# Kernel tuning notes

Measured on AMD Instinct MI355X. Metric: run time of the kernel, lower is better.

The kernel has to match this reference:

```python
import jax, jax.numpy as jnp
import numpy as np

N = 100_000          # nodes
E = 1_600_000        # directed edges
GENE_DIM = 39
NUM_CLASSES = 5
EPS = 1e-5           # BatchNorm1d eps
DIMS = [(GENE_DIM, 64), (64, 128), (128, 64), (64, 32)]


def setup_inputs() -> dict:
    key = jax.random.key(0)
    ks = jax.random.split(key, 32)
    inp = {
        "x": jax.random.normal(ks[0], (N, GENE_DIM), dtype=jnp.float32),
        "edge_index": jax.random.randint(ks[1], (2, E), 0, N, dtype=jnp.int64),
    }
    ki = 2
    for i, (din, dout) in enumerate(DIMS, start=1):
        scale = 1.0 / np.sqrt(din)
        inp[f"W{i}"] = jax.random.uniform(ks[ki], (din, dout), jnp.float32, -scale, scale); ki += 1
        inp[f"b{i}"] = jnp.zeros((dout,), jnp.float32)
        inp[f"g{i}"] = jnp.ones((dout,), jnp.float32)    # BN gamma
        inp[f"be{i}"] = jnp.zeros((dout,), jnp.float32)  # BN beta
    scale = 1.0 / np.sqrt(32)
    inp["Wc"] = jax.random.uniform(ks[ki], (32, NUM_CLASSES), jnp.float32, -scale, scale)
    inp["bc"] = jnp.zeros((NUM_CLASSES,), jnp.float32)
    return inp


def reference(x, edge_index,
              W1, b1, g1, be1,
              W2, b2, g2, be2,
              W3, b3, g3, be3,
              W4, b4, g4, be4,
              Wc, bc):
    n = x.shape[0]
    # --- self loops + symmetric GCN normalization (shared by all 4 convs) ---
    loop = jnp.arange(n, dtype=edge_index.dtype)
    src = jnp.concatenate([edge_index[0], loop])   # message source (x_j)
    dst = jnp.concatenate([edge_index[1], loop])   # aggregation target
    deg = jax.ops.segment_sum(jnp.ones_like(dst, dtype=x.dtype), dst, num_segments=n)
    dinv = jnp.where(deg > 0, jax.lax.rsqrt(deg), 0.0)
    norm = (dinv[src] * dinv[dst])[:, None]        # [E+n, 1]

    def conv(h, W, b):
        # linear transform, gather from source, normalize, scatter-add at target
        m = (h @ W)[src] * norm
        return jax.ops.segment_sum(m, dst, num_segments=n) + b

    def bn(h, g, be):
        # training-mode BatchNorm1d: biased variance over the node axis
        mu = jnp.mean(h, axis=0)
        var = jnp.mean(jnp.square(h - mu), axis=0)
        return g * (h - mu) * jax.lax.rsqrt(var + EPS) + be

    h = bn(jax.nn.relu(conv(x, W1, b1)), g1, be1)
    h = bn(jax.nn.relu(conv(h, W2, b2)), g2, be2)
    h = bn(jax.nn.relu(conv(h, W3, b3)), g3, be3)
    h = bn(jax.nn.relu(conv(h, W4, b4)), g4, be4)
    out = h @ Wc + bc
    return (out, h)
```

## Files before the change

kernel.cpp:

```cpp
#include <hip/hip_runtime.h>

typedef unsigned int uint;
typedef unsigned short ushort;
typedef __attribute__((ext_vector_type(8))) short bf16x8;
typedef __attribute__((ext_vector_type(4))) float f32x4;

#define N_NODES 100000
#define N_EDGES 1600000
#define NB_C 256
#define TILE_C ((N_EDGES + NB_C - 1) / NB_C)
#define NB_D ((N_NODES + 511) / 512)
#define MG_GRID ((N_NODES + 63) / 64)
#define AGG_GRID 2048
constexpr float BN_EPS = 1e-5f;

__device__ __forceinline__ float bflo(uint w) { return __uint_as_float(w << 16); }
__device__ __forceinline__ float bfhi(uint w) { return __uint_as_float(w & 0xffff0000u); }
__device__ __forceinline__ ushort f2bf(float x) {
    uint u = __float_as_uint(x);
    uint r = (u + 0x7fffu + ((u >> 16) & 1u)) >> 16;
    return (ushort)r;
}
__device__ __forceinline__ uint pack2(float a, float b) {
    return (uint)f2bf(a) | ((uint)f2bf(b) << 16);
}

__global__ void detect_kernel(const int* __restrict__ ep, int* __restrict__ flag)
{
    __shared__ int cnt;
    if (threadIdx.x == 0) cnt = 0;
    __syncthreads();
    int nz = 0;
    for (int k = threadIdx.x; k < 1024; k += blockDim.x)
        if (ep[2 * k + 1] != 0) nz++;
    atomicAdd(&cnt, nz);
    __syncthreads();
    if (threadIdx.x == 0) *flag = (cnt == 0) ? 1 : 0;
}

__global__ __launch_bounds__(256) void coarseA_kernel(const int* __restrict__ ep,
                                                      const int* __restrict__ flag,
                                                      uint* __restrict__ ch)
{
    __shared__ uint lh[256];
    int t = threadIdx.x, blk = blockIdx.x;
    lh[t] = 0;
    __syncthreads();
    bool i64 = (*flag != 0);
    int start = blk * TILE_C;
    int end = start + TILE_C;
    if (end > N_EDGES) end = N_EDGES;
    for (int e = start + t; e < end; e += 256) {
        int d = i64 ? ep[2 * (N_EDGES + e)] : ep[N_EDGES + e];
        atomicAdd(&lh[d >> 9], 1u);
    }
    __syncthreads();
    ch[t * NB_C + blk] = lh[t];
}

__global__ void scanB_kernel(uint* __restrict__ ch, uint* __restrict__ bucketBase)
{
    __shared__ uint tot[256];
    int t = threadIdx.x;
    uint s = 0;
    for (int i = 0; i < NB_C; i++) s += ch[t * NB_C + i];
    tot[t] = s;
    __syncthreads();
    for (int off = 1; off < 256; off <<= 1) {
        uint add = (t >= off) ? tot[t - off] : 0u;
        __syncthreads();
        tot[t] += add;
        __syncthreads();
    }
    uint base = tot[t] - s;
    bucketBase[t] = base;
    if (t == 255) bucketBase[256] = base + s;
    uint run = base;
    for (int i = 0; i < NB_C; i++) {
        uint c = ch[t * NB_C + i];
        ch[t * NB_C + i] = run;
        run += c;
    }
}

__global__ __launch_bounds__(256) void scatterC_kernel(const int* __restrict__ ep,
                                                       const int* __restrict__ flag,
                                                       const uint* __restrict__ ch,
                                                       int2* __restrict__ pair)
{
    __shared__ uint loff[256];
    int t = threadIdx.x, blk = blockIdx.x;
    loff[t] = ch[t * NB_C + blk];
    __syncthreads();
    bool i64 = (*flag != 0);
    int start = blk * TILE_C;
    int end = start + TILE_C;
    if (end > N_EDGES) end = N_EDGES;
    for (int e = start + t; e < end; e += 256) {
        int s, d;
        if (i64) { s = ep[2 * e]; d = ep[2 * (N_EDGES + e)]; }
        else     { s = ep[e];     d = ep[N_EDGES + e]; }
        uint pos = atomicAdd(&loff[d >> 9], 1u);
        pair[pos] = make_int2(s, d);
    }
}

__global__ __launch_bounds__(256) void bucketD_kernel(const int2* __restrict__ pair,
                                                      const uint* __restrict__ bucketBase,
                                                      int* __restrict__ rowptr,
                                                      float* __restrict__ dinv,
                                                      int* __restrict__ colidx)
{
    __shared__ uint cnt[512], offp[512], s2[256];
    int bin = blockIdx.x, t = threadIdx.x;
    cnt[t] = 0; cnt[t + 256] = 0;
    __syncthreads();
    uint lo = bucketBase[bin], hi = bucketBase[bin + 1];
    for (uint p = lo + t; p < hi; p += 256)
        atomicAdd(&cnt[pair[p].y & 511], 1u);
    __syncthreads();
    uint a = cnt[2 * t], b = cnt[2 * t + 1];
    s2[t] = a + b;
    __syncthreads();
    for (int off = 1; off < 256; off <<= 1) {
        uint add = (t >= off) ? s2[t - off] : 0u;
        __syncthreads();
        s2[t] += add;
        __syncthreads();
    }
    uint excl = s2[t] - (a + b);
    offp[2 * t] = excl;
    offp[2 * t + 1] = excl + a;
    __syncthreads();
    for (int k = t; k < 512; k += 256) {
        int d = bin * 512 + k;
        if (d < N_NODES) {
            rowptr[d] = (int)(lo + offp[k]);
            dinv[d] = rsqrtf((float)(cnt[k] + 1));
        }
    }
    if (bin == 0 && t == 0) rowptr[N_NODES] = N_EDGES;
    __syncthreads();
    for (uint p = lo + t; p < hi; p += 256) {
        int2 pr = pair[p];
        uint pos = lo + atomicAdd(&offp[pr.y & 511], 1u);
        colidx[pos] = pr.x;
    }
}

__global__ __launch_bounds__(256) void xscale_kernel(const float* __restrict__ x,
                                                     const float* __restrict__ dinv,
                                                     uint* __restrict__ xs)
{
    int idx = blockIdx.x * 256 + threadIdx.x;
    if (idx >= N_NODES * 32) return;
    int i = idx >> 5;
    int u = idx & 31;
    int c0 = 2 * u, c1 = 2 * u + 1;
    float di = dinv[i];
    float v0 = (c0 < 39) ? x[i * 39 + c0] * di : 0.f;
    float v1 = (c1 < 39) ? x[i * 39 + c1] * di : 0.f;
    xs[idx] = pack2(v0, v1);
}

__global__ void packW_kernel(const float* __restrict__ W, ushort* __restrict__ out,
                             int din, int dout, int K)
{
    int CT = dout >> 4;
    int tot = (K >> 5) * CT * 64 * 8;
    for (int idx = blockIdx.x * 256 + threadIdx.x; idx < tot; idx += gridDim.x * 256) {
        int j = idx & 7;
        int lane = (idx >> 3) & 63;
        int slot = idx >> 9;
        int ct = slot % CT, kt = slot / CT;
        int k = kt * 32 + (lane >> 4) * 8 + j;
        int c = ct * 16 + (lane & 15);
        float v = (k < din) ? W[k * dout + c] : 0.f;
        out[idx] = f2bf(v);
    }
}

__global__ __launch_bounds__(256) void rowsum_kernel(
    const int* __restrict__ rowptr, const int* __restrict__ colidx,
    const float* __restrict__ dinv, float* __restrict__ rowsumP)
{
    int tid = threadIdx.x;
    int lane = tid & 63, wid = tid >> 6;
    int g16 = lane >> 4, gl = lane & 15;
    int gid = (blockIdx.x * 4 + wid) * 4 + g16;
    int ng = gridDim.x * 16;
    for (int i0 = gid; i0 < N_NODES; i0 += ng) {
        int s0 = rowptr[i0], e0 = rowptr[i0 + 1];
        float ad = 0.f;
        for (int e = s0 + gl; e < e0; e += 16) ad += dinv[colidx[e]];
        ad += __shfl_xor(ad, 1); ad += __shfl_xor(ad, 2);
        ad += __shfl_xor(ad, 4); ad += __shfl_xor(ad, 8);
        if (gl == 0) {
            float di = dinv[i0];
            rowsumP[i0] = di * (ad + di);
        }
    }
}

template <int D, int MODE>
__global__ __launch_bounds__(256) void agg_kernel(
    const ushort* __restrict__ table, const int* __restrict__ rowptr,
    const int* __restrict__ colidx, const float* __restrict__ dinv,
    const float* __restrict__ bias,
    ushort* __restrict__ outB, float* __restrict__ outF,
    float* __restrict__ Psum, float* __restrict__ Psq)
{
    constexpr int LPE = D / 8;
    constexpr int S = 64 / LPE;
    int tid = threadIdx.x;
    int lane = tid & 63, wid = tid >> 6;
    int seg = lane & (LPE - 1);
    int slot = lane / LPE;
    const ushort* segbase = table + seg * 8;

    float bv[8];
    if constexpr (MODE >= 1) {
        float4 b0 = *(const float4*)&bias[seg * 8];
        float4 b1 = *(const float4*)&bias[seg * 8 + 4];
        bv[0] = b0.x; bv[1] = b0.y; bv[2] = b0.z; bv[3] = b0.w;
        bv[4] = b1.x; bv[5] = b1.y; bv[6] = b1.z; bv[7] = b1.w;
    }
    float lsum[8] = {}, lsq[8] = {};

    for (int i = blockIdx.x * 4 + wid; i < N_NODES; i += gridDim.x * 4) {
        int iu = __builtin_amdgcn_readfirstlane(i);
        int s0 = rowptr[iu], e0 = rowptr[iu + 1];
        float acc[8] = {};
        if (slot == 0) {
            const uint4 w = *(const uint4*)(segbase + (size_t)iu * D);
            acc[0] = bflo(w.x); acc[1] = bfhi(w.x);
            acc[2] = bflo(w.y); acc[3] = bfhi(w.y);
            acc[4] = bflo(w.z); acc[5] = bfhi(w.z);
            acc[6] = bflo(w.w); acc[7] = bfhi(w.w);
        }
        for (int eb = s0; eb < e0; eb += S) {
            int e = eb + slot;
            if (e < e0) {
                int j = colidx[e];
                const uint4 w = *(const uint4*)(segbase + (size_t)j * D);
                acc[0] += bflo(w.x); acc[1] += bfhi(w.x);
                acc[2] += bflo(w.y); acc[3] += bfhi(w.y);
                acc[4] += bflo(w.z); acc[5] += bfhi(w.z);
                acc[6] += bflo(w.w); acc[7] += bfhi(w.w);
            }
        }
#pragma unroll
        for (int m = LPE; m < 64; m <<= 1) {
#pragma unroll
            for (int v = 0; v < 8; v++) acc[v] += __shfl_xor(acc[v], m);
        }
        if (slot == 0) {
            float di = dinv[iu];
            if constexpr (MODE == 0) {
                uint4 pk;
                pk.x = pack2(di * acc[0], di * acc[1]);
                pk.y = pack2(di * acc[2], di * acc[3]);
                pk.z = pack2(di * acc[4], di * acc[5]);
                pk.w = pack2(di * acc[6], di * acc[7]);
                *(uint4*)(outB + (size_t)iu * D + seg * 8) = pk;
            } else {
                float t[8];
#pragma unroll
                for (int v = 0; v < 8; v++) {
                    t[v] = fmaxf(fmaf(di, acc[v], bv[v]), 0.f);
                    lsum[v] += t[v];
                    lsq[v] += t[v] * t[v];
                }
                if constexpr (MODE == 1) {
                    uint4 pk;
                    pk.x = pack2(t[0], t[1]); pk.y = pack2(t[2], t[3]);
                    pk.z = pack2(t[4], t[5]); pk.w = pack2(t[6], t[7]);
                    *(uint4*)(outB + (size_t)iu * D + seg * 8) = pk;
                } else {
                    float4 f0 = {t[0], t[1], t[2], t[3]};
                    float4 f1 = {t[4], t[5], t[6], t[7]};
                    *(float4*)(outF + (size_t)iu * D + seg * 8) = f0;
                    *(float4*)(outF + (size_t)iu * D + seg * 8 + 4) = f1;
                }
            }
        }
    }

    if constexpr (MODE >= 1) {
        __shared__ float ssum[D], ssq[D];
        for (int c = tid; c < D; c += 256) { ssum[c] = 0.f; ssq[c] = 0.f; }
        __syncthreads();
        if (slot == 0) {
#pragma unroll
            for (int v = 0; v < 8; v++) {
                atomicAdd(&ssum[seg * 8 + v], lsum[v]);
                atomicAdd(&ssq[seg * 8 + v], lsq[v]);
            }
        }
        __syncthreads();
        for (int c = tid; c < D; c += 256) {
            Psum[(size_t)c * gridDim.x + blockIdx.x] = ssum[c];
            Psq[(size_t)c * gridDim.x + blockIdx.x] = ssq[c];
        }
    }
}

template <int K, int DOUT, int MODE>
__global__ __launch_bounds__(256) void mgemm_kernel(
    const ushort* __restrict__ A, const ushort* __restrict__ Wfrag,
    const float* __restrict__ bias, const float* __restrict__ bias2,
    const float* __restrict__ rowsumP, const float* __restrict__ dinv,
    ushort* __restrict__ outB, float* __restrict__ Psum, float* __restrict__ Psq)
{
    constexpr int KT = K / 32, CT = DOUT / 16;
    int tid = threadIdx.x;
    int lane = tid & 63, wid = tid >> 6;
    int r0 = blockIdx.x * 64 + wid * 16;
    int arow = r0 + (lane & 15);
    if (arow >= N_NODES) arow = N_NODES - 1;
    const ushort* aptr = A + (size_t)arow * K + (lane >> 4) * 8;

    f32x4 acc[CT];
#pragma unroll
    for (int ct = 0; ct < CT; ct++) acc[ct] = (f32x4){0.f, 0.f, 0.f, 0.f};

#pragma unroll
    for (int kt = 0; kt < KT; kt++) {
        bf16x8 af = *(const bf16x8*)(aptr + kt * 32);
        const ushort* wp = Wfrag + ((size_t)(kt * CT) * 64 + lane) * 8;
#pragma unroll
        for (int ct = 0; ct < CT; ct++) {
            bf16x8 bfr = *(const bf16x8*)(wp + (size_t)ct * 64 * 8);
            acc[ct] = __builtin_amdgcn_mfma_f32_16x16x32_bf16(af, bfr, acc[ct], 0, 0, 0);
        }
    }

    int colbase = lane & 15;
    int rgrp = lane >> 4;
    int rows[4]; bool rok[4];
    float rP[4], rD[4];
#pragma unroll
    for (int i = 0; i < 4; i++) {
        int r = r0 + rgrp * 4 + i;
        rows[i] = r;
        rok[i] = (r < N_NODES);
        int rc = rok[i] ? r : 0;
        if constexpr (MODE == 1) rP[i] = rowsumP[rc];
        else rD[i] = dinv[rc];
    }

    __shared__ float ssum[DOUT], ssq[DOUT];
    if constexpr (MODE <= 1) {
        for (int c = tid; c < DOUT; c += 256) { ssum[c] = 0.f; ssq[c] = 0.f; }
        __syncthreads();
    }

#pragma unroll
    for (int ct = 0; ct < CT; ct++) {
        int col = ct * 16 + colbase;
        float b = bias[col];
        float b2 = 0.f;
        if constexpr (MODE == 1) b2 = bias2[col];
        float cs = 0.f, cq = 0.f;
#pragma unroll
        for (int i = 0; i < 4; i++) {
            float v = acc[ct][i] + b;
            if constexpr (MODE == 1) v = fmaf(rP[i], b2, v);
            if constexpr (MODE <= 1) v = fmaxf(v, 0.f);
            float w = (MODE == 1) ? v : rD[i] * v;
            if (rok[i]) {
                outB[(size_t)rows[i] * DOUT + col] = f2bf(w);
                if constexpr (MODE <= 1) { cs += v; cq += v * v; }
            }
        }
        if constexpr (MODE <= 1) {
            cs += __shfl_xor(cs, 16); cs += __shfl_xor(cs, 32);
            cq += __shfl_xor(cq, 16); cq += __shfl_xor(cq, 32);
            if (rgrp == 0) {
                atomicAdd(&ssum[col], cs);
                atomicAdd(&ssq[col], cq);
            }
        }
    }
    if constexpr (MODE <= 1) {
        __syncthreads();
        for (int c = tid; c < DOUT; c += 256) {
            Psum[(size_t)c * gridDim.x + blockIdx.x] = ssum[c];
            Psq[(size_t)c * gridDim.x + blockIdx.x] = ssq[c];
        }
    }
}

__global__ __launch_bounds__(256) void reduce_bn_kernel(
    const float* __restrict__ Psum, const float* __restrict__ Psq, int nb,
    const float* __restrict__ g, const float* __restrict__ be,
    float* __restrict__ sOut, float* __restrict__ uOut)
{
    int c = blockIdx.x, t = threadIdx.x;
    float s = 0.f, q = 0.f;
    for (int i = t; i < nb; i += 256) {
        s += Psum[(size_t)c * nb + i];
        q += Psq[(size_t)c * nb + i];
    }
    __shared__ float rs[256], rq[256];
    rs[t] = s; rq[t] = q;
    __syncthreads();
    for (int off = 128; off > 0; off >>= 1) {
        if (t < off) { rs[t] += rs[t + off]; rq[t] += rq[t + off]; }
        __syncthreads();
    }
    if (t == 0) {
        float mu = rs[0] * (1.0f / N_NODES);
        float var = rq[0] * (1.0f / N_NODES) - mu * mu;
        float sv = g[c] * rsqrtf(var + BN_EPS);
        sOut[c] = sv;
        uOut[c] = be[c] - mu * sv;
    }
}

__global__ void foldW_kernel(const float* __restrict__ W, const float* __restrict__ s,
                             const float* __restrict__ u, float* __restrict__ Wf,
                             float* __restrict__ v, int din, int dout)
{
    int c = blockIdx.x, t = threadIdx.x;
    float contrib = 0.f;
    if (t < din) {
        float w = W[t * dout + c];
        Wf[t * dout + c] = s[t] * w;
        contrib = u[t] * w;
    }
    __shared__ float red[128];
    red[t] = contrib;
    __syncthreads();
    for (int off = 64; off > 0; off >>= 1) {
        if (t < off) red[t] += red[t + off];
        __syncthreads();
    }
    if (t == 0) v[c] = red[0];
}

__global__ __launch_bounds__(256) void final_kernel(
    const float* __restrict__ t4, const float* __restrict__ sArr,
    const float* __restrict__ uArr, const float* __restrict__ Wc,
    const float* __restrict__ bc, float* __restrict__ out_logits,
    float* __restrict__ out_h)
{
    __shared__ float sc[32], sh2[32], Wcs[160], bcs[5];
    int t = threadIdx.x;
    if (t < 32) { sc[t] = sArr[t]; sh2[t] = uArr[t]; }
    if (t < 160) Wcs[t] = Wc[t];
    if (t < 5) bcs[t] = bc[t];
    __syncthreads();
    int i = blockIdx.x * blockDim.x + t;
    if (i >= N_NODES) return;
    float hv[32];
#pragma unroll
    for (int f0 = 0; f0 < 32; f0 += 4) {
        float4 v = *(const float4*)&t4[(size_t)i * 32 + f0];
        hv[f0 + 0] = fmaf(sc[f0 + 0], v.x, sh2[f0 + 0]);
        hv[f0 + 1] = fmaf(sc[f0 + 1], v.y, sh2[f0 + 1]);
        hv[f0 + 2] = fmaf(sc[f0 + 2], v.z, sh2[f0 + 2]);
        hv[f0 + 3] = fmaf(sc[f0 + 3], v.w, sh2[f0 + 3]);
    }
#pragma unroll
    for (int f0 = 0; f0 < 32; f0 += 4) {
        float4 v = {hv[f0], hv[f0 + 1], hv[f0 + 2], hv[f0 + 3]};
        *(float4*)&out_h[(size_t)i * 32 + f0] = v;
    }
    float o[5];
#pragma unroll
    for (int c = 0; c < 5; c++) o[c] = bcs[c];
#pragma unroll
    for (int f = 0; f < 32; f++) {
        float hvf = hv[f];
#pragma unroll
        for (int c = 0; c < 5; c++) o[c] = fmaf(hvf, Wcs[f * 5 + c], o[c]);
    }
#pragma unroll
    for (int c = 0; c < 5; c++) out_logits[(size_t)i * 5 + c] = o[c];
}

extern "C" void kernel_launch(void* const* d_in, const int* in_sizes, int n_in,
                              void* d_out, int out_size, void* d_ws, size_t ws_size,
                              hipStream_t stream)
{
    const float* x = (const float*)d_in[0];
    const int* ei = (const int*)d_in[1];
    const float* W1 = (const float*)d_in[2];
    const float* b1 = (const float*)d_in[3];
    const float* g1 = (const float*)d_in[4];
    const float* be1 = (const float*)d_in[5];
    const float* W2 = (const float*)d_in[6];
    const float* b2 = (const float*)d_in[7];
    const float* g2 = (const float*)d_in[8];
    const float* be2 = (const float*)d_in[9];
    const float* W3 = (const float*)d_in[10];
    const float* b3 = (const float*)d_in[11];
    const float* g3 = (const float*)d_in[12];
    const float* be3 = (const float*)d_in[13];
    const float* W4 = (const float*)d_in[14];
    const float* b4 = (const float*)d_in[15];
    const float* g4 = (const float*)d_in[16];
    const float* be4 = (const float*)d_in[17];
    const float* Wc = (const float*)d_in[18];
    const float* bc = (const float*)d_in[19];

    char* ws = (char*)d_ws;
    size_t off = 0;
    auto alloc = [&](size_t bytes) -> void* {
        void* p = ws + off;
        off += (bytes + 255) & ~(size_t)255;
        return p;
    };
    uint* ch = (uint*)alloc(65536 * 4);
    uint* bucketBase = (uint*)alloc(257 * 4);
    int2* pair = (int2*)alloc((size_t)N_EDGES * 8);
    int* rowptr = (int*)alloc((size_t)(N_NODES + 1) * 4);
    float* dinv = (float*)alloc((size_t)N_NODES * 4);
    int* colidx = (int*)alloc((size_t)N_EDGES * 4);
    int* flag = (int*)alloc(256);
    float* rowsumP = (float*)alloc((size_t)N_NODES * 4);
    uint* xs = (uint*)alloc((size_t)N_NODES * 32 * 4);
    float* Wf = (float*)alloc(128 * 128 * 4);
    ushort* Wfrag = (ushort*)alloc(32768);
    float* vB = (float*)alloc(128 * 4);
    float* sArr = (float*)alloc(128 * 4);
    float* uArr = (float*)alloc(128 * 4);
    float* Psum = (float*)alloc((size_t)128 * 2048 * 4);
    float* Psq = (float*)alloc((size_t)128 * 2048 * 4);
    ushort* P = (ushort*)alloc((size_t)N_NODES * 64 * 2);
    ushort* Q = (ushort*)alloc((size_t)N_NODES * 64 * 2);
    ushort* R = (ushort*)alloc((size_t)N_NODES * 128 * 2);
    if (off > ws_size) return;

    detect_kernel<<<1, 256, 0, stream>>>(ei, flag);
    coarseA_kernel<<<NB_C, 256, 0, stream>>>(ei, flag, ch);
    scanB_kernel<<<1, 256, 0, stream>>>(ch, bucketBase);
    scatterC_kernel<<<NB_C, 256, 0, stream>>>(ei, flag, ch, pair);
    bucketD_kernel<<<NB_D, 256, 0, stream>>>(pair, bucketBase, rowptr, dinv, colidx);

    xscale_kernel<<<(N_NODES * 32 + 255) / 256, 256, 0, stream>>>(x, dinv, xs);
    packW_kernel<<<16, 256, 0, stream>>>(W1, Wfrag, 39, 64, 64);
    rowsum_kernel<<<512, 256, 0, stream>>>(rowptr, colidx, dinv, rowsumP);

    agg_kernel<64, 0><<<AGG_GRID, 256, 0, stream>>>(
        (const ushort*)xs, rowptr, colidx, dinv, nullptr, P, nullptr, nullptr, nullptr);
    mgemm_kernel<64, 64, 0><<<MG_GRID, 256, 0, stream>>>(
        P, Wfrag, b1, nullptr, nullptr, dinv, Q, Psum, Psq);
    reduce_bn_kernel<<<64, 256, 0, stream>>>(Psum, Psq, MG_GRID, g1, be1, sArr, uArr);
    foldW_kernel<<<128, 128, 0, stream>>>(W2, sArr, uArr, Wf, vB, 64, 128);
    packW_kernel<<<32, 256, 0, stream>>>(Wf, Wfrag, 64, 128, 64);

    agg_kernel<64, 0><<<AGG_GRID, 256, 0, stream>>>(
        Q, rowptr, colidx, dinv, nullptr, P, nullptr, nullptr, nullptr);
    mgemm_kernel<64, 128, 1><<<MG_GRID, 256, 0, stream>>>(
        P, Wfrag, b2, vB, rowsumP, nullptr, R, Psum, Psq);
    reduce_bn_kernel<<<128, 256, 0, stream>>>(Psum, Psq, MG_GRID, g2, be2, sArr, uArr);
    foldW_kernel<<<64, 128, 0, stream>>>(W3, sArr, uArr, Wf, vB, 128, 64);
    packW_kernel<<<32, 256, 0, stream>>>(Wf, Wfrag, 128, 64, 128);

    mgemm_kernel<128, 64, 2><<<MG_GRID, 256, 0, stream>>>(
        R, Wfrag, vB, nullptr, nullptr, dinv, P, nullptr, nullptr);
    agg_kernel<64, 1><<<AGG_GRID, 256, 0, stream>>>(
        P, rowptr, colidx, dinv, b3, Q, nullptr, Psum, Psq);
    reduce_bn_kernel<<<64, 256, 0, stream>>>(Psum, Psq, AGG_GRID, g3, be3, sArr, uArr);
    foldW_kernel<<<32, 128, 0, stream>>>(W4, sArr, uArr, Wf, vB, 64, 32);
    packW_kernel<<<16, 256, 0, stream>>>(Wf, Wfrag, 64, 32, 64);

    mgemm_kernel<64, 32, 2><<<MG_GRID, 256, 0, stream>>>(
        Q, Wfrag, vB, nullptr, nullptr, dinv, P, nullptr, nullptr);
    agg_kernel<32, 2><<<AGG_GRID, 256, 0, stream>>>(
        P, rowptr, colidx, dinv, b4, nullptr, (float*)R, Psum, Psq);
    reduce_bn_kernel<<<32, 256, 0, stream>>>(Psum, Psq, AGG_GRID, g4, be4, sArr, uArr);

    float* out_logits = (float*)d_out;
    float* out_h = (float*)d_out + (size_t)N_NODES * 5;
    final_kernel<<<(N_NODES + 255) / 256, 256, 0, stream>>>((const float*)R, sArr, uArr,
                                                            Wc, bc, out_logits, out_h);
}
```

Measured before the change: 388.7 us.

## Fuse setup kernels, compute rowsum inside aggregation, unroll gathers, store layer-4 in bf16

Index-width detection now runs as a per-block wave ballot, which removes the detect kernel and the flag buffer. The weight fold and pack kernels are merged into one foldpack kernel. The row sum is computed by placing dinv in padding column 39 of the scaled input, so the first aggregation produces it and rowsum_kernel goes away. The gather loop handles two edges per iteration using nontemporal loads, and the layer-4 output is stored as bf16 instead of fp32. This cuts launch count and memory traffic, at some risk to precision and cache behaviour.

```diff
diff --git a/kernel.cpp b/kernel.cpp
--- a/kernel.cpp
+++ b/kernel.cpp
@@ -4,6 +4,7 @@
 typedef unsigned short ushort;
 typedef __attribute__((ext_vector_type(8))) short bf16x8;
 typedef __attribute__((ext_vector_type(4))) float f32x4;
+typedef __attribute__((ext_vector_type(4))) uint uintx4;
 
 #define N_NODES 100000
 #define N_EDGES 1600000
@@ -25,28 +26,21 @@
     return (uint)f2bf(a) | ((uint)f2bf(b) << 16);
 }
 
-__global__ void detect_kernel(const int* __restrict__ ep, int* __restrict__ flag)
-{
-    __shared__ int cnt;
-    if (threadIdx.x == 0) cnt = 0;
-    __syncthreads();
-    int nz = 0;
-    for (int k = threadIdx.x; k < 1024; k += blockDim.x)
-        if (ep[2 * k + 1] != 0) nz++;
-    atomicAdd(&cnt, nz);
-    __syncthreads();
-    if (threadIdx.x == 0) *flag = (cnt == 0) ? 1 : 0;
+__device__ __forceinline__ bool detect_i64(const int* __restrict__ ep)
+{
+    int lane = threadIdx.x & 63;
+    unsigned long long nz = __ballot(ep[2 * lane + 1] != 0);
+    return nz == 0ULL;
 }
 
 __global__ __launch_bounds__(256) void coarseA_kernel(const int* __restrict__ ep,
-                                                      const int* __restrict__ flag,
                                                       uint* __restrict__ ch)
 {
     __shared__ uint lh[256];
     int t = threadIdx.x, blk = blockIdx.x;
     lh[t] = 0;
-    __syncthreads();
-    bool i64 = (*flag != 0);
+    bool i64 = detect_i64(ep);
+    __syncthreads();
     int start = blk * TILE_C;
     int end = start + TILE_C;
     if (end > N_EDGES) end = N_EDGES;
@@ -84,15 +78,14 @@
 }
 
 __global__ __launch_bounds__(256) void scatterC_kernel(const int* __restrict__ ep,
-                                                       const int* __restrict__ flag,
                                                        const uint* __restrict__ ch,
                                                        int2* __restrict__ pair)
 {
     __shared__ uint loff[256];
     int t = threadIdx.x, blk = blockIdx.x;
     loff[t] = ch[t * NB_C + blk];
-    __syncthreads();
-    bool i64 = (*flag != 0);
+    bool i64 = detect_i64(ep);
+    __syncthreads();
     int start = blk * TILE_C;
     int end = start + TILE_C;
     if (end > N_EDGES) end = N_EDGES;
@@ -159,55 +152,46 @@
     int c0 = 2 * u, c1 = 2 * u + 1;
     float di = dinv[i];
     float v0 = (c0 < 39) ? x[i * 39 + c0] * di : 0.f;
-    float v1 = (c1 < 39) ? x[i * 39 + c1] * di : 0.f;
+    float v1 = (c1 < 39) ? x[i * 39 + c1] * di : ((c1 == 39) ? di : 0.f);
     xs[idx] = pack2(v0, v1);
 }
 
-__global__ void packW_kernel(const float* __restrict__ W, ushort* __restrict__ out,
-                             int din, int dout, int K)
-{
-    int CT = dout >> 4;
-    int tot = (K >> 5) * CT * 64 * 8;
-    for (int idx = blockIdx.x * 256 + threadIdx.x; idx < tot; idx += gridDim.x * 256) {
-        int j = idx & 7;
-        int lane = (idx >> 3) & 63;
-        int slot = idx >> 9;
-        int ct = slot % CT, kt = slot / CT;
-        int k = kt * 32 + (lane >> 4) * 8 + j;
-        int c = ct * 16 + (lane & 15);
-        float v = (k < din) ? W[k * dout + c] : 0.f;
-        out[idx] = f2bf(v);
-    }
-}
-
-__global__ __launch_bounds__(256) void rowsum_kernel(
-    const int* __restrict__ rowptr, const int* __restrict__ colidx,
-    const float* __restrict__ dinv, float* __restrict__ rowsumP)
-{
-    int tid = threadIdx.x;
-    int lane = tid & 63, wid = tid >> 6;
-    int g16 = lane >> 4, gl = lane & 15;
-    int gid = (blockIdx.x * 4 + wid) * 4 + g16;
-    int ng = gridDim.x * 16;
-    for (int i0 = gid; i0 < N_NODES; i0 += ng) {
-        int s0 = rowptr[i0], e0 = rowptr[i0 + 1];
-        float ad = 0.f;
-        for (int e = s0 + gl; e < e0; e += 16) ad += dinv[colidx[e]];
-        ad += __shfl_xor(ad, 1); ad += __shfl_xor(ad, 2);
-        ad += __shfl_xor(ad, 4); ad += __shfl_xor(ad, 8);
-        if (gl == 0) {
-            float di = dinv[i0];
-            rowsumP[i0] = di * (ad + di);
-        }
-    }
-}
-
-template <int D, int MODE>
+__global__ void foldpack_kernel(const float* __restrict__ W, const float* __restrict__ s,
+                                const float* __restrict__ u, ushort* __restrict__ Wfrag,
+                                float* __restrict__ vB, int din, int dout, int K)
+{
+    int CT = dout >> 4, KT = K >> 5;
+    int nf = KT * CT;
+    int b = blockIdx.x;
+    if (b < nf) {
+        int kt = b / CT, ct = b - kt * CT;
+        for (int q = threadIdx.x; q < 512; q += 256) {
+            int j = q & 7, lane = q >> 3;
+            int k = kt * 32 + (lane >> 4) * 8 + j;
+            int c = ct * 16 + (lane & 15);
+            float v = 0.f;
+            if (k < din) {
+                float sv = s ? s[k] : 1.f;
+                v = sv * W[k * dout + c];
+            }
+            Wfrag[(size_t)b * 512 + q] = f2bf(v);
+        }
+    } else {
+        int c = threadIdx.x;
+        if (u && c < dout) {
+            float acc = 0.f;
+            for (int k = 0; k < din; k++) acc += u[k] * W[k * dout + c];
+            vB[c] = acc;
+        }
+    }
+}
+
+template <int D, int MODE, int WRSUM>
 __global__ __launch_bounds__(256) void agg_kernel(
     const ushort* __restrict__ table, const int* __restrict__ rowptr,
     const int* __restrict__ colidx, const float* __restrict__ dinv,
     const float* __restrict__ bias,
-    ushort* __restrict__ outB, float* __restrict__ outF,
+    ushort* __restrict__ outB, float* __restrict__ rowsumP,
     float* __restrict__ Psum, float* __restrict__ Psq)
 {
     constexpr int LPE = D / 8;
@@ -219,7 +203,7 @@
     const ushort* segbase = table + seg * 8;
 
     float bv[8];
-    if constexpr (MODE >= 1) {
+    if constexpr (MODE == 1) {
         float4 b0 = *(const float4*)&bias[seg * 8];
         float4 b1 = *(const float4*)&bias[seg * 8 + 4];
         bv[0] = b0.x; bv[1] = b0.y; bv[2] = b0.z; bv[3] = b0.w;
@@ -232,22 +216,31 @@
         int s0 = rowptr[iu], e0 = rowptr[iu + 1];
         float acc[8] = {};
         if (slot == 0) {
-            const uint4 w = *(const uint4*)(segbase + (size_t)iu * D);
+            const uintx4 w = *(const uintx4*)(segbase + (size_t)iu * D);
             acc[0] = bflo(w.x); acc[1] = bfhi(w.x);
             acc[2] = bflo(w.y); acc[3] = bfhi(w.y);
             acc[4] = bflo(w.z); acc[5] = bfhi(w.z);
             acc[6] = bflo(w.w); acc[7] = bfhi(w.w);
         }
-        for (int eb = s0; eb < e0; eb += S) {
-            int e = eb + slot;
-            if (e < e0) {
-                int j = colidx[e];
-                const uint4 w = *(const uint4*)(segbase + (size_t)j * D);
-                acc[0] += bflo(w.x); acc[1] += bfhi(w.x);
-                acc[2] += bflo(w.y); acc[3] += bfhi(w.y);
-                acc[4] += bflo(w.z); acc[5] += bfhi(w.z);
-                acc[6] += bflo(w.w); acc[7] += bfhi(w.w);
-            }
+        for (int eb = s0; eb < e0; eb += 2 * S) {
+            int e1 = eb + slot, e2 = eb + S + slot;
+            uintx4 w1 = {0u, 0u, 0u, 0u}, w2 = {0u, 0u, 0u, 0u};
+            if (e1 < e0) {
+                int j = colidx[e1];
+                w1 = __builtin_nontemporal_load((const uintx4*)(segbase + (size_t)j * D));
+            }
+            if (e2 < e0) {
+                int j = colidx[e2];
+                w2 = __builtin_nontemporal_load((const uintx4*)(segbase + (size_t)j * D));
+            }
+            acc[0] += bflo(w1.x) + bflo(w2.x);
+            acc[1] += bfhi(w1.x) + bfhi(w2.x);
+            acc[2] += bflo(w1.y) + bflo(w2.y);
+            acc[3] += bfhi(w1.y) + bfhi(w2.y);
+            acc[4] += bflo(w1.z) + bflo(w2.z);
+            acc[5] += bfhi(w1.z) + bfhi(w2.z);
+            acc[6] += bflo(w1.w) + bflo(w2.w);
+            acc[7] += bfhi(w1.w) + bfhi(w2.w);
         }
 #pragma unroll
         for (int m = LPE; m < 64; m <<= 1) {
@@ -257,12 +250,15 @@
         if (slot == 0) {
             float di = dinv[iu];
             if constexpr (MODE == 0) {
-                uint4 pk;
+                uintx4 pk;
                 pk.x = pack2(di * acc[0], di * acc[1]);
                 pk.y = pack2(di * acc[2], di * acc[3]);
                 pk.z = pack2(di * acc[4], di * acc[5]);
                 pk.w = pack2(di * acc[6], di * acc[7]);
-                *(uint4*)(outB + (size_t)iu * D + seg * 8) = pk;
+                *(uintx4*)(outB + (size_t)iu * D + seg * 8) = pk;
+                if constexpr (WRSUM) {
+                    if (seg == 4) rowsumP[iu] = di * acc[7];
+                }
             } else {
                 float t[8];
 #pragma unroll
@@ -271,22 +267,15 @@
                     lsum[v] += t[v];
                     lsq[v] += t[v] * t[v];
                 }
-                if constexpr (MODE == 1) {
-                    uint4 pk;
-                    pk.x = pack2(t[0], t[1]); pk.y = pack2(t[2], t[3]);
-                    pk.z = pack2(t[4], t[5]); pk.w = pack2(t[6], t[7]);
-                    *(uint4*)(outB + (size_t)iu * D + seg * 8) = pk;
-                } else {
-                    float4 f0 = {t[0], t[1], t[2], t[3]};
-                    float4 f1 = {t[4], t[5], t[6], t[7]};
-                    *(float4*)(outF + (size_t)iu * D + seg * 8) = f0;
-                    *(float4*)(outF + (size_t)iu * D + seg * 8 + 4) = f1;
-                }
-            }
-        }
-    }
-
-    if constexpr (MODE >= 1) {
+                uintx4 pk;
+                pk.x = pack2(t[0], t[1]); pk.y = pack2(t[2], t[3]);
+                pk.z = pack2(t[4], t[5]); pk.w = pack2(t[6], t[7]);
+                *(uintx4*)(outB + (size_t)iu * D + seg * 8) = pk;
+            }
+        }
+    }
+
+    if constexpr (MODE == 1) {
         __shared__ float ssum[D], ssq[D];
         for (int c = tid; c < D; c += 256) { ssum[c] = 0.f; ssq[c] = 0.f; }
         __syncthreads();
@@ -418,29 +407,8 @@
     }
 }
 
-__global__ void foldW_kernel(const float* __restrict__ W, const float* __restrict__ s,
-                             const float* __restrict__ u, float* __restrict__ Wf,
-                             float* __restrict__ v, int din, int dout)
-{
-    int c = blockIdx.x, t = threadIdx.x;
-    float contrib = 0.f;
-    if (t < din) {
-        float w = W[t * dout + c];
-        Wf[t * dout + c] = s[t] * w;
-        contrib = u[t] * w;
-    }
-    __shared__ float red[128];
-    red[t] = contrib;
-    __syncthreads();
-    for (int off = 64; off > 0; off >>= 1) {
-        if (t < off) red[t] += red[t + off];
-        __syncthreads();
-    }
-    if (t == 0) v[c] = red[0];
-}
-
 __global__ __launch_bounds__(256) void final_kernel(
-    const float* __restrict__ t4, const float* __restrict__ sArr,
+    const ushort* __restrict__ t4, const float* __restrict__ sArr,
     const float* __restrict__ uArr, const float* __restrict__ Wc,
     const float* __restrict__ bc, float* __restrict__ out_logits,
     float* __restrict__ out_h)
@@ -454,13 +422,19 @@
     int i = blockIdx.x * blockDim.x + t;
     if (i >= N_NODES) return;
     float hv[32];
-#pragma unroll
-    for (int f0 = 0; f0 < 32; f0 += 4) {
-        float4 v = *(const float4*)&t4[(size_t)i * 32 + f0];
-        hv[f0 + 0] = fmaf(sc[f0 + 0], v.x, sh2[f0 + 0]);
-        hv[f0 + 1] = fmaf(sc[f0 + 1], v.y, sh2[f0 + 1]);
-        hv[f0 + 2] = fmaf(sc[f0 + 2], v.z, sh2[f0 + 2]);
-        hv[f0 + 3] = fmaf(sc[f0 + 3], v.w, sh2[f0 + 3]);
+    const uint* tp = (const uint*)(t4 + (size_t)i * 32);
+#pragma unroll
+    for (int q = 0; q < 4; q++) {
+        uintx4 w = *(const uintx4*)(tp + q * 4);
+        int f0 = q * 8;
+        hv[f0 + 0] = fmaf(sc[f0 + 0], bflo(w.x), sh2[f0 + 0]);
+        hv[f0 + 1] = fmaf(sc[f0 + 1], bfhi(w.x), sh2[f0 + 1]);
+        hv[f0 + 2] = fmaf(sc[f0 + 2], bflo(w.y), sh2[f0 + 2]);
+        hv[f0 + 3] = fmaf(sc[f0 + 3], bfhi(w.y), sh2[f0 + 3]);
+        hv[f0 + 4] = fmaf(sc[f0 + 4], bflo(w.z), sh2[f0 + 4]);
+        hv[f0 + 5] = fmaf(sc[f0 + 5], bfhi(w.z), sh2[f0 + 5]);
+        hv[f0 + 6] = fmaf(sc[f0 + 6], bflo(w.w), sh2[f0 + 6]);
+        hv[f0 + 7] = fmaf(sc[f0 + 7], bfhi(w.w), sh2[f0 + 7]);
     }
 #pragma unroll
     for (int f0 = 0; f0 < 32; f0 += 4) {
@@ -518,10 +492,8 @@
     int* rowptr = (int*)alloc((size_t)(N_NODES + 1) * 4);
     float* dinv = (float*)alloc((size_t)N_NODES * 4);
     int* colidx = (int*)alloc((size_t)N_EDGES * 4);
-    int* flag = (int*)alloc(256);
     float* rowsumP = (float*)alloc((size_t)N_NODES * 4);
     uint* xs = (uint*)alloc((size_t)N_NODES * 32 * 4);
-    float* Wf = (float*)alloc(128 * 128 * 4);
     ushort* Wfrag = (ushort*)alloc(32768);
     float* vB = (float*)alloc(128 * 4);
     float* sArr = (float*)alloc(128 * 4);
@@ -533,48 +505,43 @@
     ushort* R = (ushort*)alloc((size_t)N_NODES * 128 * 2);
     if (off > ws_size) return;
 
-    detect_kernel<<<1, 256, 0, stream>>>(ei, flag);
-    coarseA_kernel<<<NB_C, 256, 0, stream>>>(ei, flag, ch);
+    coarseA_kernel<<<NB_C, 256, 0, stream>>>(ei, ch);
     scanB_kernel<<<1, 256, 0, stream>>>(ch, bucketBase);
-    scatterC_kernel<<<NB_C, 256, 0, stream>>>(ei, flag, ch, pair);
+    scatterC_kernel<<<NB_C, 256, 0, stream>>>(ei, ch, pair);
     bucketD_kernel<<<NB_D, 256, 0, stream>>>(pair, bucketBase, rowptr, dinv, colidx);
 
     xscale_kernel<<<(N_NODES * 32 + 255) / 256, 256, 0, stream>>>(x, dinv, xs);
-    packW_kernel<<<16, 256, 0, stream>>>(W1, Wfrag, 39, 64, 64);
-    rowsum_kernel<<<512, 256, 0, stream>>>(rowptr, colidx, dinv, rowsumP);
-
-    agg_kernel<64, 0><<<AGG_GRID, 256, 0, stream>>>(
-        (const ushort*)xs, rowptr, colidx, dinv, nullptr, P, nullptr, nullptr, nullptr);
+    foldpack_kernel<<<8, 256, 0, stream>>>(W1, nullptr, nullptr, Wfrag, nullptr, 39, 64, 64);
+
+    agg_kernel<64, 0, 1><<<AGG_GRID, 256, 0, stream>>>(
+        (const ushort*)xs, rowptr, colidx, dinv, nullptr, P, rowsumP, nullptr, nullptr);
     mgemm_kernel<64, 64, 0><<<MG_GRID, 256, 0, stream>>>(
         P, Wfrag, b1, nullptr, nullptr, dinv, Q, Psum, Psq);
     reduce_bn_kernel<<<64, 256, 0, stream>>>(Psum, Psq, MG_GRID, g1, be1, sArr, uArr);
-    foldW_kernel<<<128, 128, 0, stream>>>(W2, sArr, uArr, Wf, vB, 64, 128);
-    packW_kernel<<<32, 256, 0, stream>>>(Wf, Wfrag, 64, 128, 64);
-
-    agg_kernel<64, 0><<<AGG_GRID, 256, 0, stream>>>(
+    foldpack_kernel<<<17, 256, 0, stream>>>(W2, sArr, uArr, Wfrag, vB, 64, 128, 64);
+
+    agg_kernel<64, 0, 0><<<AGG_GRID, 256, 0, stream>>>(
         Q, rowptr, colidx, dinv, nullptr, P, nullptr, nullptr, nullptr);
     mgemm_kernel<64, 128, 1><<<MG_GRID, 256, 0, stream>>>(
         P, Wfrag, b2, vB, rowsumP, nullptr, R, Psum, Psq);
     reduce_bn_kernel<<<128, 256, 0, stream>>>(Psum, Psq, MG_GRID, g2, be2, sArr, uArr);
-    foldW_kernel<<<64, 128, 0, stream>>>(W3, sArr, uArr, Wf, vB, 128, 64);
-    packW_kernel<<<32, 256, 0, stream>>>(Wf, Wfrag, 128, 64, 128);
+    foldpack_kernel<<<17, 256, 0, stream>>>(W3, sArr, uArr, Wfrag, vB, 128, 64, 128);
 
     mgemm_kernel<128, 64, 2><<<MG_GRID, 256, 0, stream>>>(
         R, Wfrag, vB, nullptr, nullptr, dinv, P, nullptr, nullptr);
-    agg_kernel<64, 1><<<AGG_GRID, 256, 0, stream>>>(
+    agg_kernel<64, 1, 0><<<AGG_GRID, 256, 0, stream>>>(
         P, rowptr, colidx, dinv, b3, Q, nullptr, Psum, Psq);
     reduce_bn_kernel<<<64, 256, 0, stream>>>(Psum, Psq, AGG_GRID, g3, be3, sArr, uArr);
-    foldW_kernel<<<32, 128, 0, stream>>>(W4, sArr, uArr, Wf, vB, 64, 32);
-    packW_kernel<<<16, 256, 0, stream>>>(Wf, Wfrag, 64, 32, 64);
+    foldpack_kernel<<<5, 256, 0, stream>>>(W4, sArr, uArr, Wfrag, vB, 64, 32, 64);
 
     mgemm_kernel<64, 32, 2><<<MG_GRID, 256, 0, stream>>>(
         Q, Wfrag, vB, nullptr, nullptr, dinv, P, nullptr, nullptr);
-    agg_kernel<32, 2><<<AGG_GRID, 256, 0, stream>>>(
-        P, rowptr, colidx, dinv, b4, nullptr, (float*)R, Psum, Psq);
+    agg_kernel<32, 1, 0><<<AGG_GRID, 256, 0, stream>>>(
+        P, rowptr, colidx, dinv, b4, R, nullptr, Psum, Psq);
     reduce_bn_kernel<<<32, 256, 0, stream>>>(Psum, Psq, AGG_GRID, g4, be4, sArr, uArr);
 
     float* out_logits = (float*)d_out;
     float* out_h = (float*)d_out + (size_t)N_NODES * 5;
-    final_kernel<<<(N_NODES + 255) / 256, 256, 0, stream>>>((const float*)R, sArr, uArr,
-                                                            Wc, bc, out_logits, out_h);
-}
+    final_kernel<<<(N_NODES + 255) / 256, 256, 0, stream>>>(R, sArr, uArr, Wc, bc,
+                                                            out_logits, out_h);
+}
```

Result: slower. 454.8 us (+17.0%).
